# Performance work log

Measured on AMD Instinct MI355X. Metric: run time of the kernel, lower is better.

The kernel has to match this reference:

```python
import jax, jax.numpy as jnp
import numpy as np

N, C, C_OUT, E = 50000, 128, 256, 600000


def setup_inputs() -> dict:
    key = jax.random.key(0)
    k1, k2, k3, k4, k5 = jax.random.split(key, 5)
    x = jax.random.normal(k1, (N, C), dtype=jnp.float32)
    edge_index = jax.random.randint(k2, (2, E), 0, N, dtype=jnp.int64)
    # torch Linear(2C -> C_OUT): weight [out, in], bias [out]
    bound = 1.0 / np.sqrt(2 * C)
    W = jax.random.uniform(k3, (C_OUT, 2 * C), dtype=jnp.float32, minval=-bound, maxval=bound)
    b = jax.random.uniform(k4, (C_OUT,), dtype=jnp.float32, minval=-bound, maxval=bound)
    return {"x": x, "edge_index": edge_index, "W": W, "b": b}


def reference(x, edge_index, W, b):
    src, dst = edge_index[0], edge_index[1]
    # gather - subtract: relative features per edge [E, C]
    rel = x[src] - x[dst]
    # scatter-max into destination nodes; empty segments -> 0 (torch_scatter fill)
    x_j = jax.ops.segment_max(rel, dst, num_segments=N)
    x_j = jnp.where(jnp.isfinite(x_j), x_j, 0.0)
    # concat + Linear + ReLU (MLP([2C, C_OUT], act='relu'))
    h = jnp.concatenate([x, x_j], axis=1)  # [N, 2C]
    out = h @ W.T + b
    return jax.nn.relu(out)
```

## Files before the change

kernel.cpp:

```cpp
#include <hip/hip_runtime.h>

#define NNODES 50000
#define CIN    128
#define COUT   256
#define KTOT   256

typedef float  f32x4  __attribute__((ext_vector_type(4)));
typedef short  bf16x8 __attribute__((ext_vector_type(8)));

#define GLOAD16(gptr, lptr) __builtin_amdgcn_global_load_lds(                      \
    (const __attribute__((address_space(1))) void*)(gptr),                         \
    (__attribute__((address_space(3))) void*)(lptr), 16, 0, 0)

__device__ __forceinline__ unsigned short f2bf(float f) {
    union { float f; unsigned int u; } v; v.f = f;
    unsigned int r = v.u + 0x7FFFu + ((v.u >> 16) & 1u);
    return (unsigned short)(r >> 16);
}
__device__ __forceinline__ float bf2f(unsigned short u) {
    return __uint_as_float((unsigned int)u << 16);
}

#define PREP_X   1600000
#define PREP_C   1650000
#define PREP_W   1666384

__global__ __launch_bounds__(256)
void prep_kernel(const float* __restrict__ x, const float* __restrict__ W,
                 unsigned short* __restrict__ xcat, unsigned short* __restrict__ Wbf,
                 int* __restrict__ cnt) {
    int g = blockIdx.x * 256 + threadIdx.x;
    if (g < PREP_X) {
        float4 v = ((const float4*)x)[g];
        int row = g >> 5;
        int col = (g & 31) * 4;
        *(ushort4*)(xcat + (size_t)row * KTOT + col) =
            make_ushort4(f2bf(v.x), f2bf(v.y), f2bf(v.z), f2bf(v.w));
    } else if (g < PREP_C) {
        cnt[g - PREP_X] = 0;
    } else if (g < PREP_W) {
        int i = g - PREP_C;
        float4 v = ((const float4*)W)[i];
        *(ushort4*)(Wbf + (size_t)i * 4) =
            make_ushort4(f2bf(v.x), f2bf(v.y), f2bf(v.z), f2bf(v.w));
    }
}

__global__ void hist_kernel(const int* __restrict__ dst, int* __restrict__ cnt, int E) {
    int i = blockIdx.x * blockDim.x + threadIdx.x;
    if (i < E) atomicAdd(&cnt[dst[i]], 1);
}

__global__ __launch_bounds__(1024)
void scan_onepass(const int* __restrict__ cnt, int* __restrict__ row_start) {
    __shared__ int tile[4096];
    __shared__ int tsum[1024];
    const int tid = threadIdx.x;
    int carry = 0;

    for (int c0 = 0; c0 < NNODES; c0 += 4096) {
#pragma unroll
        for (int j = 0; j < 4; ++j) {
            int idx = c0 + j * 1024 + tid;
            tile[j * 1024 + tid] = (idx < NNODES) ? cnt[idx] : 0;
        }
        __syncthreads();
        int a0 = tile[tid * 4 + 0], a1 = tile[tid * 4 + 1];
        int a2 = tile[tid * 4 + 2], a3 = tile[tid * 4 + 3];
        int s = a0 + a1 + a2 + a3;
        tsum[tid] = s;
        __syncthreads();
        for (int off = 1; off < 1024; off <<= 1) {
            int t = (tid >= off) ? tsum[tid - off] : 0;
            __syncthreads();
            tsum[tid] += t;
            __syncthreads();
        }
        int excl = tsum[tid] - s + carry;
        int chunktot = tsum[1023];
        int base = c0 + tid * 4;
        if (base < NNODES) {
            *(int4*)&row_start[base] = make_int4(excl, excl + a0, excl + a0 + a1,
                                                 excl + a0 + a1 + a2);
        }
        carry += chunktot;
    }
    if (tid == 0) row_start[NNODES] = carry;
}

__global__ void scatter_kernel(const int* __restrict__ src, const int* __restrict__ dst,
                               const int* __restrict__ row_start, int* __restrict__ cnt,
                               int* __restrict__ sorted_src, int E) {
    int i = blockIdx.x * blockDim.x + threadIdx.x;
    if (i < E) {
        int d = dst[i];
        int pos = atomicSub(&cnt[d], 1) - 1;
        sorted_src[row_start[d] + pos] = src[i];
    }
}

__device__ __forceinline__ float2 fmax2(float2 a, float2 b) {
    return make_float2(fmaxf(a.x, b.x), fmaxf(a.y, b.y));
}

__global__ __launch_bounds__(256)
void gather_max_kernel(const float* __restrict__ x,
                       const int* __restrict__ row_start,
                       const int* __restrict__ sorted_src,
                       unsigned short* __restrict__ xcat) {
    int wid  = (blockIdx.x * blockDim.x + threadIdx.x) >> 6;
    int lane = threadIdx.x & 63;
    if (wid >= NNODES) return;

    int start = row_start[wid];
    int end   = row_start[wid + 1];

    const float NI = __int_as_float(0xFF800000u);
    float2 m0 = make_float2(NI, NI), m1 = m0, m2 = m0, m3 = m0;

    int t = start;
    for (; t + 4 <= end; t += 4) {
        int s0 = sorted_src[t + 0];
        int s1 = sorted_src[t + 1];
        int s2 = sorted_src[t + 2];
        int s3 = sorted_src[t + 3];
        ushort2 u0 = *(const ushort2*)(xcat + (size_t)s0 * KTOT + lane * 2);
        ushort2 u1 = *(const ushort2*)(xcat + (size_t)s1 * KTOT + lane * 2);
        ushort2 u2 = *(const ushort2*)(xcat + (size_t)s2 * KTOT + lane * 2);
        ushort2 u3 = *(const ushort2*)(xcat + (size_t)s3 * KTOT + lane * 2);
        m0 = fmax2(m0, make_float2(bf2f(u0.x), bf2f(u0.y)));
        m1 = fmax2(m1, make_float2(bf2f(u1.x), bf2f(u1.y)));
        m2 = fmax2(m2, make_float2(bf2f(u2.x), bf2f(u2.y)));
        m3 = fmax2(m3, make_float2(bf2f(u3.x), bf2f(u3.y)));
    }
    for (; t < end; ++t) {
        int s = sorted_src[t];
        ushort2 u = *(const ushort2*)(xcat + (size_t)s * KTOT + lane * 2);
        m0 = fmax2(m0, make_float2(bf2f(u.x), bf2f(u.y)));
    }
    float2 mx = fmax2(fmax2(m0, m1), fmax2(m2, m3));

    float2 xv = ((const float2*)(x + (size_t)wid * CIN))[lane];
    bool nonempty = (end > start);
    float2 o;
    o.x = nonempty ? mx.x - xv.x : 0.0f;
    o.y = nonempty ? mx.y - xv.y : 0.0f;
    *((ushort2*)(xcat + (size_t)wid * KTOT + CIN + lane * 2)) =
        make_ushort2(f2bf(o.x), f2bf(o.y));
}

__global__ __launch_bounds__(256, 3)
void mfma_gemm(const unsigned short* __restrict__ xcat,
               const unsigned short* __restrict__ Wbf,
               const float* __restrict__ bias,
               float* __restrict__ out) {
    __shared__ unsigned short As[2][64][32];
    __shared__ unsigned short Bs[2][256][32];

    const int M = NNODES;
    const int m0 = blockIdx.x * 64;

    const int tid  = threadIdx.x;
    const int lane = tid & 63;
    const int wid  = tid >> 6;

    f32x4 acc[4][4] = {};

    auto stage = [&](int b, int kt) {
        {
            int row  = tid >> 2;
            int kseg = (tid & 3) * 8;
            int grow = m0 + row; if (grow > M - 1) grow = M - 1;
            GLOAD16(xcat + (size_t)grow * KTOT + kt + kseg, &As[b][row][kseg]);
        }
#pragma unroll
        for (int j = 0; j < 4; ++j) {
            int u    = j * 256 + tid;
            int row  = u >> 2;
            int kseg = (u & 3) * 8;
            GLOAD16(Wbf + (size_t)row * KTOT + kt + kseg, &Bs[b][row][kseg]);
        }
    };

    stage(0, 0);
    __syncthreads();

    const int l15 = lane & 15;
    const int kh  = (lane >> 4) * 8;

#pragma unroll
    for (int t = 0; t < 8; ++t) {
        int b = t & 1;
        if (t < 7) stage(b ^ 1, (t + 1) * 32);

        bf16x8 af[4], bfr[4];
#pragma unroll
        for (int m = 0; m < 4; ++m)
            af[m] = *(const bf16x8*)&As[b][m * 16 + l15][kh];
#pragma unroll
        for (int n = 0; n < 4; ++n)
            bfr[n] = *(const bf16x8*)&Bs[b][wid * 64 + n * 16 + l15][kh];
#pragma unroll
        for (int m = 0; m < 4; ++m)
#pragma unroll
            for (int n = 0; n < 4; ++n)
                acc[m][n] = __builtin_amdgcn_mfma_f32_16x16x32_bf16(af[m], bfr[n], acc[m][n], 0, 0, 0);

        __syncthreads();
    }

#pragma unroll
    for (int n = 0; n < 4; ++n) {
        int col = wid * 64 + n * 16 + l15;
        float bv = bias[col];
#pragma unroll
        for (int m = 0; m < 4; ++m) {
            int r0 = m0 + m * 16 + ((lane >> 4) << 2);
            f32x4 a = acc[m][n];
#pragma unroll
            for (int r = 0; r < 4; ++r) {
                int rr = r0 + r;
                if (rr < M) out[(size_t)rr * COUT + col] = fmaxf(a[r] + bv, 0.0f);
            }
        }
    }
}

extern "C" void kernel_launch(void* const* d_in, const int* in_sizes, int n_in,
                              void* d_out, int out_size, void* d_ws, size_t ws_size,
                              hipStream_t stream) {
    const float* x  = (const float*)d_in[0];
    const int*   ei = (const int*)d_in[1];
    const float* W  = (const float*)d_in[2];
    const float* b  = (const float*)d_in[3];
    float*       out = (float*)d_out;

    const int E = in_sizes[1] / 2;
    const int* src = ei;
    const int* dst = ei + E;

    unsigned short* xcat       = (unsigned short*)d_ws;
    unsigned short* Wbf        = xcat + (size_t)NNODES * KTOT;
    int*            cnt        = (int*)(Wbf + COUT * KTOT);
    int*            row_start  = cnt + NNODES;
    int*            sorted_src = row_start + (NNODES + 1);

    const int NB_E = (E + 255) / 256;

    prep_kernel<<<(PREP_W + 255) / 256, 256, 0, stream>>>(x, W, xcat, Wbf, cnt);
    hist_kernel<<<NB_E, 256, 0, stream>>>(dst, cnt, E);
    scan_onepass<<<1, 1024, 0, stream>>>(cnt, row_start);
    scatter_kernel<<<NB_E, 256, 0, stream>>>(src, dst, row_start, cnt, sorted_src, E);
    gather_max_kernel<<<(NNODES * 64 + 255) / 256, 256, 0, stream>>>(x, row_start, sorted_src, xcat);
    mfma_gemm<<<(NNODES + 63) / 64, 256, 0, stream>>>(xcat, Wbf, b, out);
}
```

Baseline: 234.9 us.

## Parallelize scan across blocks, deepen gather unroll, swizzle GEMM LDS tiles

```diff
diff --git a/kernel.cpp b/kernel.cpp
--- a/kernel.cpp
+++ b/kernel.cpp
@@ -51,41 +51,49 @@
     if (i < E) atomicAdd(&cnt[dst[i]], 1);
 }
 
-__global__ __launch_bounds__(1024)
-void scan_onepass(const int* __restrict__ cnt, int* __restrict__ row_start) {
-    __shared__ int tile[4096];
-    __shared__ int tsum[1024];
+__global__ __launch_bounds__(256)
+void scan_partial(const int* __restrict__ cnt, int* __restrict__ partial, int n) {
+    __shared__ int s[256];
+    int tid = threadIdx.x;
+    int i = blockIdx.x * 256 + tid;
+    s[tid] = (i < n) ? cnt[i] : 0;
+    __syncthreads();
+    for (int off = 128; off > 0; off >>= 1) {
+        if (tid < off) s[tid] += s[tid + off];
+        __syncthreads();
+    }
+    if (tid == 0) partial[blockIdx.x] = s[0];
+}
+
+__global__ __launch_bounds__(256)
+void scan_final(const int* __restrict__ cnt, const int* __restrict__ partial,
+                int* __restrict__ row_start, int nb) {
+    __shared__ int ps[256];
+    __shared__ int s[256];
     const int tid = threadIdx.x;
-    int carry = 0;
-
-    for (int c0 = 0; c0 < NNODES; c0 += 4096) {
-#pragma unroll
-        for (int j = 0; j < 4; ++j) {
-            int idx = c0 + j * 1024 + tid;
-            tile[j * 1024 + tid] = (idx < NNODES) ? cnt[idx] : 0;
-        }
-        __syncthreads();
-        int a0 = tile[tid * 4 + 0], a1 = tile[tid * 4 + 1];
-        int a2 = tile[tid * 4 + 2], a3 = tile[tid * 4 + 3];
-        int s = a0 + a1 + a2 + a3;
-        tsum[tid] = s;
-        __syncthreads();
-        for (int off = 1; off < 1024; off <<= 1) {
-            int t = (tid >= off) ? tsum[tid - off] : 0;
-            __syncthreads();
-            tsum[tid] += t;
-            __syncthreads();
-        }
-        int excl = tsum[tid] - s + carry;
-        int chunktot = tsum[1023];
-        int base = c0 + tid * 4;
-        if (base < NNODES) {
-            *(int4*)&row_start[base] = make_int4(excl, excl + a0, excl + a0 + a1,
-                                                 excl + a0 + a1 + a2);
-        }
-        carry += chunktot;
-    }
-    if (tid == 0) row_start[NNODES] = carry;
+
+    ps[tid] = (tid < nb) ? partial[tid] : 0;
+    __syncthreads();
+    for (int off = 1; off < 256; off <<= 1) {
+        int t = (tid >= off) ? ps[tid - off] : 0;
+        __syncthreads();
+        ps[tid] += t;
+        __syncthreads();
+    }
+    int base = (blockIdx.x == 0) ? 0 : ps[blockIdx.x - 1];
+
+    int i = blockIdx.x * 256 + tid;
+    int v = (i < NNODES) ? cnt[i] : 0;
+    s[tid] = v;
+    __syncthreads();
+    for (int off = 1; off < 256; off <<= 1) {
+        int t = (tid >= off) ? s[tid - off] : 0;
+        __syncthreads();
+        s[tid] += t;
+        __syncthreads();
+    }
+    if (i < NNODES) row_start[i] = base + s[tid] - v;
+    if (i == NNODES - 1) row_start[NNODES] = base + s[tid];
 }
 
 __global__ void scatter_kernel(const int* __restrict__ src, const int* __restrict__ dst,
@@ -116,29 +124,30 @@
     int end   = row_start[wid + 1];
 
     const float NI = __int_as_float(0xFF800000u);
-    float2 m0 = make_float2(NI, NI), m1 = m0, m2 = m0, m3 = m0;
+    float2 mm[8];
+#pragma unroll
+    for (int j = 0; j < 8; ++j) mm[j] = make_float2(NI, NI);
 
     int t = start;
-    for (; t + 4 <= end; t += 4) {
-        int s0 = sorted_src[t + 0];
-        int s1 = sorted_src[t + 1];
-        int s2 = sorted_src[t + 2];
-        int s3 = sorted_src[t + 3];
-        ushort2 u0 = *(const ushort2*)(xcat + (size_t)s0 * KTOT + lane * 2);
-        ushort2 u1 = *(const ushort2*)(xcat + (size_t)s1 * KTOT + lane * 2);
-        ushort2 u2 = *(const ushort2*)(xcat + (size_t)s2 * KTOT + lane * 2);
-        ushort2 u3 = *(const ushort2*)(xcat + (size_t)s3 * KTOT + lane * 2);
-        m0 = fmax2(m0, make_float2(bf2f(u0.x), bf2f(u0.y)));
-        m1 = fmax2(m1, make_float2(bf2f(u1.x), bf2f(u1.y)));
-        m2 = fmax2(m2, make_float2(bf2f(u2.x), bf2f(u2.y)));
-        m3 = fmax2(m3, make_float2(bf2f(u3.x), bf2f(u3.y)));
+    for (; t + 8 <= end; t += 8) {
+        int     si[8];
+        ushort2 uu[8];
+#pragma unroll
+        for (int j = 0; j < 8; ++j) si[j] = sorted_src[t + j];
+#pragma unroll
+        for (int j = 0; j < 8; ++j)
+            uu[j] = *(const ushort2*)(xcat + (size_t)si[j] * KTOT + lane * 2);
+#pragma unroll
+        for (int j = 0; j < 8; ++j)
+            mm[j] = fmax2(mm[j], make_float2(bf2f(uu[j].x), bf2f(uu[j].y)));
     }
     for (; t < end; ++t) {
         int s = sorted_src[t];
         ushort2 u = *(const ushort2*)(xcat + (size_t)s * KTOT + lane * 2);
-        m0 = fmax2(m0, make_float2(bf2f(u.x), bf2f(u.y)));
-    }
-    float2 mx = fmax2(fmax2(m0, m1), fmax2(m2, m3));
+        mm[0] = fmax2(mm[0], make_float2(bf2f(u.x), bf2f(u.y)));
+    }
+    float2 mx = fmax2(fmax2(fmax2(mm[0], mm[1]), fmax2(mm[2], mm[3])),
+                      fmax2(fmax2(mm[4], mm[5]), fmax2(mm[6], mm[7])));
 
     float2 xv = ((const float2*)(x + (size_t)wid * CIN))[lane];
     bool nonempty = (end > start);
@@ -170,15 +179,17 @@
         {
             int row  = tid >> 2;
             int kseg = (tid & 3) * 8;
+            int ks   = kseg ^ ((row & 3) << 3);
             int grow = m0 + row; if (grow > M - 1) grow = M - 1;
-            GLOAD16(xcat + (size_t)grow * KTOT + kt + kseg, &As[b][row][kseg]);
+            GLOAD16(xcat + (size_t)grow * KTOT + kt + ks, &As[b][row][kseg]);
         }
 #pragma unroll
         for (int j = 0; j < 4; ++j) {
             int u    = j * 256 + tid;
             int row  = u >> 2;
             int kseg = (u & 3) * 8;
-            GLOAD16(Wbf + (size_t)row * KTOT + kt + kseg, &Bs[b][row][kseg]);
+            int ks   = kseg ^ ((row & 3) << 3);
+            GLOAD16(Wbf + (size_t)row * KTOT + kt + ks, &Bs[b][row][kseg]);
         }
     };
 
@@ -187,6 +198,7 @@
 
     const int l15 = lane & 15;
     const int kh  = (lane >> 4) * 8;
+    const int khs = kh ^ ((l15 & 3) << 3);
 
 #pragma unroll
     for (int t = 0; t < 8; ++t) {
@@ -196,10 +208,10 @@
         bf16x8 af[4], bfr[4];
 #pragma unroll
         for (int m = 0; m < 4; ++m)
-            af[m] = *(const bf16x8*)&As[b][m * 16 + l15][kh];
+            af[m] = *(const bf16x8*)&As[b][m * 16 + l15][khs];
 #pragma unroll
         for (int n = 0; n < 4; ++n)
-            bfr[n] = *(const bf16x8*)&Bs[b][wid * 64 + n * 16 + l15][kh];
+            bfr[n] = *(const bf16x8*)&Bs[b][wid * 64 + n * 16 + l15][khs];
 #pragma unroll
         for (int m = 0; m < 4; ++m)
 #pragma unroll
@@ -244,12 +256,15 @@
     int*            cnt        = (int*)(Wbf + COUT * KTOT);
     int*            row_start  = cnt + NNODES;
     int*            sorted_src = row_start + (NNODES + 1);
-
+    int*            partial    = sorted_src + E;
+
+    const int NB_N = (NNODES + 255) / 256;
     const int NB_E = (E + 255) / 256;
 
     prep_kernel<<<(PREP_W + 255) / 256, 256, 0, stream>>>(x, W, xcat, Wbf, cnt);
     hist_kernel<<<NB_E, 256, 0, stream>>>(dst, cnt, E);
-    scan_onepass<<<1, 1024, 0, stream>>>(cnt, row_start);
+    scan_partial<<<NB_N, 256, 0, stream>>>(cnt, partial, NNODES);
+    scan_final<<<NB_N, 256, 0, stream>>>(cnt, partial, row_start, NB_N);
     scatter_kernel<<<NB_E, 256, 0, stream>>>(src, dst, row_start, cnt, sorted_src, E);
     gather_max_kernel<<<(NNODES * 64 + 255) / 256, 256, 0, stream>>>(x, row_start, sorted_src, xcat);
     mfma_gemm<<<(NNODES + 63) / 64, 256, 0, stream>>>(xcat, Wbf, b, out);
```

Result: faster. 208.7 us (-11.2%).
